# Optimization experiments

Measured on AMD Instinct MI355X. Metric: run time of the kernel, lower is better.

Reference implementation:

```python
import jax, jax.numpy as jnp
import numpy as np

B, T, D = 32, 2000, 1024

def setup_inputs() -> dict:
    key = jax.random.key(0)
    # drive with positive mean current so neurons actually spike
    I_seq = 100.0 * jax.random.normal(key, (B, T, D), dtype=jnp.float32) + 250.0
    C, g_L, E_L, V_T, Delta_T, tau_w = 200.0, 10.0, -70.0, -50.0, 2.0, 120.0
    a, b, R, V_reset, V_spike, dt = 0.0, 0.0, 1.0, -65.0, 30.0, 0.1
    tau_m = C / max(1e-06, g_L)
    params = jnp.array([tau_m, E_L, V_T, Delta_T, R, tau_w, a, b, V_reset, V_spike, dt],
                       dtype=jnp.float32)
    return {"I_seq": I_seq, "params": params}


def reference(I_seq, params):
    tau_m, E_L, V_T, Delta_T, R, tau_w, a, b, V_reset, V_spike, dt = params
    Bs, Ts, Ds = I_seq.shape
    # flatten to (T, B*D): scan over time, all neurons vectorized
    flat_I = jnp.transpose(I_seq, (1, 0, 2)).reshape(Ts, Bs * Ds)
    V0 = jnp.full((Bs * Ds,), E_L, dtype=I_seq.dtype)
    w0 = jnp.zeros((Bs * Ds,), dtype=I_seq.dtype)

    def step(carry, i_t):
        V, w = carry
        exp_term = Delta_T * jnp.exp((V - V_T) / Delta_T)
        dV = (-(V - E_L) + exp_term - R * w + R * i_t) / tau_m
        V = V + dt * dV
        dw = (a * (V - E_L) - w) / tau_w
        w = w + dt * dw
        spk = (V >= V_spike).astype(V.dtype)
        V = jnp.where(spk > 0.0, V_reset, V)
        w = jnp.where(spk > 0.0, w + b, w)
        return (V, w), spk

    (_, _), spikes = jax.lax.scan(step, (V0, w0), flat_I)  # spikes: (T, B*D)
    return jnp.transpose(spikes.reshape(Ts, Bs, Ds), (1, 0, 2))  # (B, T, D)
```

## Files before the change

kernel.cpp:

```cpp
#include <hip/hip_runtime.h>


#define Bn 32
#define Tn 2000
#define Dn 1024
#define NEUR (Bn * Dn)
#define UNR 16
#define NB (Tn / UNR)

#define EXP_LOG2EF 1.44269504088896341f
#define EXP_C1 0.693359375f
#define EXP_C2 -2.12194440e-4f
#define EXP_P0 1.9875691500e-4f
#define EXP_P1 1.3981999507e-3f
#define EXP_P2 8.3334519073e-3f
#define EXP_P3 4.1665795894e-2f
#define EXP_P4 1.6666665459e-1f
#define EXP_P5 5.0000001201e-1f

__device__ __forceinline__ float ref_expf(float x) {
    #pragma clang fp contract(off)
    float fx = __builtin_floorf(__builtin_fmaf(x, EXP_LOG2EF, 0.5f));
    float xr = __builtin_fmaf(fx, -EXP_C1, x);
    xr = __builtin_fmaf(fx, -EXP_C2, xr);
    float z2 = xr * xr;
    float y = EXP_P0;
    y = __builtin_fmaf(y, xr, EXP_P1);
    y = __builtin_fmaf(y, xr, EXP_P2);
    y = __builtin_fmaf(y, xr, EXP_P3);
    y = __builtin_fmaf(y, xr, EXP_P4);
    y = __builtin_fmaf(y, xr, EXP_P5);
    y = __builtin_fmaf(y, z2, xr);
    y = y + 1.0f;
    const int n = (int)fx;
    return y * __int_as_float((n + 127) << 23);
}

struct HP {
    float tau_m, rTM, dt, Vs, Vrst, E_L, V_T;
    float rDT;
    float KH;
    float T1C;
    float nC;
    int   kdt;
};

__device__ __forceinline__ float hot_step(float& V, float& t1, float& nEL,
                                          float i_t, const HP p) {
    #pragma clang fp contract(off)
    const float x  = t1 * p.rDT;
    const float fx = __builtin_floorf(__builtin_fmaf(t1, p.KH, 0.5f));
    float xr = __builtin_fmaf(fx, -EXP_C1, x);
    xr = __builtin_fmaf(fx, -EXP_C2, xr);
    const float z2 = xr * xr;
    float y = __builtin_fmaf(EXP_P0, xr, EXP_P1);
    y = __builtin_fmaf(y, xr, EXP_P2);
    y = __builtin_fmaf(y, xr, EXP_P3);
    y = __builtin_fmaf(y, xr, EXP_P4);
    y = __builtin_fmaf(y, xr, EXP_P5);
    y = __builtin_fmaf(y, z2, xr);
    y = y + 1.0f;
    const int   nsc = (int)fx;
    const float sc  = __int_as_float((nsc + 127 + p.kdt) << 23);
    const float et  = y * sc;
    float nm = nEL + et;
    nm = nm + i_t;
    const float q  = nm * p.rTM;
    const float er = __builtin_fmaf(-p.tau_m, q, nm);
    const float dV = __builtin_fmaf(er, p.rTM, q);
    const float Vp = __builtin_fmaf(p.dt, dV, V);
    const bool  s  = (Vp >= p.Vs);
    V   = s ? p.Vrst : Vp;
    t1  = s ? p.T1C  : (Vp - p.V_T);
    nEL = s ? p.nC   : (p.E_L - Vp);
    return s ? 1.0f : 0.0f;
}

__device__ __forceinline__ void step_simple(float& V, float i_t, float& spk_out,
                                            float E_L, float V_T, float Delta_T,
                                            float R, float tau_m, float V_spike,
                                            float V_reset, float dt) {
    #pragma clang fp contract(off)
    const float e  = ref_expf((V - V_T) / Delta_T);
    const float et = Delta_T * e;
    float nm = (-(V - E_L) + et);
    nm = nm + R * i_t;
    const float dV = nm / tau_m;
    V = __builtin_fmaf(dt, dV, V);
    spk_out = (V >= V_spike) ? 1.0f : 0.0f;
    V = (V >= V_spike) ? V_reset : V;
}

__device__ __forceinline__ void step_general(float& V, float& w, float i_t, float& spk_out,
                                             float E_L, float V_T, float Delta_T,
                                             float R, float tau_m, float tau_w,
                                             float a, float b,
                                             float V_spike, float V_reset, float dt) {
    #pragma clang fp contract(off)
    const float e  = ref_expf((V - V_T) / Delta_T);
    const float et = Delta_T * e;
    float nm = (-(V - E_L) + et);
    nm = __builtin_fmaf(-R, w, nm);
    nm = __builtin_fmaf(R, i_t, nm);
    const float dV = nm / tau_m;
    V = __builtin_fmaf(dt, dV, V);
    const float dwn = __builtin_fmaf(a, (V - E_L), -w);
    const float dw  = dwn / tau_w;
    w = __builtin_fmaf(dt, dw, w);
    spk_out = (V >= V_spike) ? 1.0f : 0.0f;
    const bool s = (V >= V_spike);
    V = s ? V_reset : V;
    w = s ? (w + b) : w;
}

#define RUN_BLOCKS(IPTR, OPTR, NBLK, ...) do {                                    \
    float bufA_[UNR], bufB_[UNR];                                                 \
    _Pragma("unroll") for (int k = 0; k < UNR; ++k) bufA_[k] = (IPTR)[k * Dn];    \
    for (int tb = 0; tb < (NBLK); tb += 2) {                                      \
        if (tb + 1 < (NBLK)) {                                                    \
            const float* pp_ = (IPTR) + (size_t)(tb + 1) * (UNR * Dn);            \
            _Pragma("unroll") for (int k = 0; k < UNR; ++k) bufB_[k] = pp_[k*Dn]; \
        }                                                                         \
        {                                                                         \
            float* oo_ = (OPTR) + (size_t)tb * (UNR * Dn);                        \
            _Pragma("unroll") for (int k = 0; k < UNR; ++k) {                     \
                const float i_t = bufA_[k];                                       \
                float* OSLOT = oo_ + (size_t)k * Dn; (void)OSLOT;                 \
                __VA_ARGS__;                                                      \
            }                                                                     \
        }                                                                         \
        if (tb + 2 < (NBLK)) {                                                    \
            const float* pp_ = (IPTR) + (size_t)(tb + 2) * (UNR * Dn);            \
            _Pragma("unroll") for (int k = 0; k < UNR; ++k) bufA_[k] = pp_[k*Dn]; \
        }                                                                         \
        if (tb + 1 < (NBLK)) {                                                    \
            float* oo_ = (OPTR) + (size_t)(tb + 1) * (UNR * Dn);                  \
            _Pragma("unroll") for (int k = 0; k < UNR; ++k) {                     \
                const float i_t = bufB_[k];                                       \
                float* OSLOT = oo_ + (size_t)k * Dn; (void)OSLOT;                 \
                __VA_ARGS__;                                                      \
            }                                                                     \
        }                                                                         \
    }                                                                             \
} while (0)

__launch_bounds__(128, 1)
__global__ void adex_kernel(const float* __restrict__ I,
                            const float* __restrict__ params,
                            float* __restrict__ out) {
    #pragma clang fp contract(off)

    const float tau_m   = params[0];
    const float E_L     = params[1];
    const float V_T     = params[2];
    const float Delta_T = params[3];
    const float R       = params[4];
    const float tau_w   = params[5];
    const float a       = params[6];
    const float b       = params[7];
    const float V_reset = params[8];
    const float V_spike = params[9];
    const float dt      = params[10];

    const int n = blockIdx.x * blockDim.x + threadIdx.x;
    if (n >= NEUR) return;
    const int bb = n >> 10;
    const int dd = n & (Dn - 1);

    const float* Ip = I   + (size_t)bb * (size_t)(Tn * Dn) + dd;
    float*       Op = out + (size_t)bb * (size_t)(Tn * Dn) + dd;

    const unsigned dtBits = __float_as_uint(Delta_T);
    const bool dtPow2 = ((dtBits & 0x7FFFFFu) == 0u) && Delta_T > 0.0f;
    const bool hot = (a == 0.0f) && (b == 0.0f) && (R == 1.0f) && dtPow2;

    float V = E_L;

    if (hot) {
        HP p;
        p.tau_m = tau_m;
        p.rTM   = 1.0f / tau_m;
        p.dt    = dt;
        p.Vs    = V_spike;
        p.Vrst  = V_reset;
        p.E_L   = E_L;
        p.V_T   = V_T;
        p.kdt   = (int)((dtBits >> 23) & 0xFFu) - 127;
        p.rDT   = 1.0f / Delta_T;
        p.KH    = EXP_LOG2EF * p.rDT;
        p.T1C   = V_reset - V_T;
        p.nC    = E_L - V_reset;

        float t1  = V - V_T;
        float nEL = E_L - V;
        RUN_BLOCKS(Ip, Op, NB,
            { *OSLOT = hot_step(V, t1, nEL, i_t, p); });
    } else if (a == 0.0f && b == 0.0f) {
        RUN_BLOCKS(Ip, Op, NB,
            { float spk; step_simple(V, i_t, spk, E_L, V_T, Delta_T, R, tau_m,
                                     V_spike, V_reset, dt); *OSLOT = spk; });
    } else {
        float w = 0.0f;
        RUN_BLOCKS(Ip, Op, NB,
            { float spk; step_general(V, w, i_t, spk, E_L, V_T, Delta_T, R, tau_m,
                                      tau_w, a, b, V_spike, V_reset, dt); *OSLOT = spk; });
    }
}

extern "C" void kernel_launch(void* const* d_in, const int* in_sizes, int n_in,
                              void* d_out, int out_size, void* d_ws, size_t ws_size,
                              hipStream_t stream) {
    const float* I      = (const float*)d_in[0];
    const float* params = (const float*)d_in[1];
    float*       out    = (float*)d_out;

    dim3 block(128);
    dim3 grid(NEUR / 128);
    adex_kernel<<<grid, block, 0, stream>>>(I, params, out);
}
```

Before: 190.2 us.

## Precompute post-reset step to shorten serial dependency chain in hot path

Restructures the hot-path recurrence so that the step following a spike uses a precomputed constant exponential term (the value at V_reset). The candidate post-reset voltage is computed in parallel with the general step, and a select picks between them. This takes the reset select off the critical path before the exp polynomial. It also inlines an explicit double-buffered prefetch of input blocks in place of the RUN_BLOCKS macro. The exp is still evaluated every step, so arithmetic work rises a little in exchange for a shorter dependency latency.

```diff
diff --git a/kernel.cpp b/kernel.cpp
--- a/kernel.cpp
+++ b/kernel.cpp
@@ -36,20 +36,10 @@
     return y * __int_as_float((n + 127) << 23);
 }
 
-struct HP {
-    float tau_m, rTM, dt, Vs, Vrst, E_L, V_T;
-    float rDT;
-    float KH;
-    float T1C;
-    float nC;
-    int   kdt;
-};
-
-__device__ __forceinline__ float hot_step(float& V, float& t1, float& nEL,
-                                          float i_t, const HP p) {
-    #pragma clang fp contract(off)
-    const float x  = t1 * p.rDT;
-    const float fx = __builtin_floorf(__builtin_fmaf(t1, p.KH, 0.5f));
+__device__ __forceinline__ float et_from_t1(float t1, float rDT, float KH, int kdt) {
+    #pragma clang fp contract(off)
+    const float x  = t1 * rDT;
+    const float fx = __builtin_floorf(__builtin_fmaf(t1, KH, 0.5f));
     float xr = __builtin_fmaf(fx, -EXP_C1, x);
     xr = __builtin_fmaf(fx, -EXP_C2, xr);
     const float z2 = xr * xr;
@@ -60,20 +50,8 @@
     y = __builtin_fmaf(y, xr, EXP_P5);
     y = __builtin_fmaf(y, z2, xr);
     y = y + 1.0f;
-    const int   nsc = (int)fx;
-    const float sc  = __int_as_float((nsc + 127 + p.kdt) << 23);
-    const float et  = y * sc;
-    float nm = nEL + et;
-    nm = nm + i_t;
-    const float q  = nm * p.rTM;
-    const float er = __builtin_fmaf(-p.tau_m, q, nm);
-    const float dV = __builtin_fmaf(er, p.rTM, q);
-    const float Vp = __builtin_fmaf(p.dt, dV, V);
-    const bool  s  = (Vp >= p.Vs);
-    V   = s ? p.Vrst : Vp;
-    t1  = s ? p.T1C  : (Vp - p.V_T);
-    nEL = s ? p.nC   : (p.E_L - Vp);
-    return s ? 1.0f : 0.0f;
+    const int nsc = (int)fx;
+    return y * __int_as_float((nsc + 127 + kdt) << 23);
 }
 
 __device__ __forceinline__ void step_simple(float& V, float i_t, float& spk_out,
@@ -174,28 +152,91 @@
     const bool dtPow2 = ((dtBits & 0x7FFFFFu) == 0u) && Delta_T > 0.0f;
     const bool hot = (a == 0.0f) && (b == 0.0f) && (R == 1.0f) && dtPow2;
 
+    if (hot) {
+        const int   kdt = (int)((dtBits >> 23) & 0xFFu) - 127;
+        const float rDT = 1.0f / Delta_T;
+        const float KH  = EXP_LOG2EF * rDT;
+        const float rTM = 1.0f / tau_m;
+        const float t1C  = V_reset - V_T;
+        const float etC  = et_from_t1(t1C, rDT, KH, kdt);
+        const float nC   = E_L - V_reset;
+        const float nmC0 = nC + etC;
+
+        float VP = E_L;
+        bool  s  = false;
+
+        float bufA[UNR], bufB[UNR], sp[UNR];
+        #pragma unroll
+        for (int k = 0; k < UNR; ++k) bufA[k] = Ip[k * Dn];
+
+        #define HOT_STEP(i_t, kk) do {                                            \
+                               \
+            const float nms = nmC0 + (i_t);                                       \
+            const float qs  = nms * rTM;                                          \
+            const float ers = __builtin_fmaf(-tau_m, qs, nms);                    \
+            const float dVs = __builtin_fmaf(ers, rTM, qs);                       \
+            const float Vs_ = __builtin_fmaf(dt, dVs, V_reset);                   \
+                  \
+            const float t1 = VP - V_T;                                            \
+            const float x  = t1 * rDT;                                            \
+            const float fx = __builtin_floorf(__builtin_fmaf(t1, KH, 0.5f));      \
+            float xr = __builtin_fmaf(fx, -EXP_C1, x);                            \
+            xr = __builtin_fmaf(fx, -EXP_C2, xr);                                 \
+            const float z2 = xr * xr;                                             \
+            float y = __builtin_fmaf(EXP_P0, xr, EXP_P1);                         \
+            y = __builtin_fmaf(y, xr, EXP_P2);                                    \
+            y = __builtin_fmaf(y, xr, EXP_P3);                                    \
+            y = __builtin_fmaf(y, xr, EXP_P4);                                    \
+            y = __builtin_fmaf(y, xr, EXP_P5);                                    \
+            y = __builtin_fmaf(y, z2, xr);                                        \
+            y = y + 1.0f;                                                         \
+            const int   nsc = (int)fx;                                            \
+            const float sc  = __int_as_float((nsc + 127 + kdt) << 23);            \
+            const float et  = y * sc;                                             \
+            const float nEL = E_L - VP;                                           \
+            float nm = nEL + et;                                                  \
+            nm = nm + (i_t);                                                      \
+            const float q  = nm * rTM;                                            \
+            const float er = __builtin_fmaf(-tau_m, q, nm);                       \
+            const float dV = __builtin_fmaf(er, rTM, q);                          \
+            const float Vns = __builtin_fmaf(dt, dV, VP);                         \
+            VP = s ? Vs_ : Vns;                       \
+            s  = (VP >= V_spike);               \
+            sp[kk] = s ? 1.0f : 0.0f;                                             \
+        } while (0)
+
+        for (int tb = 0; tb < NB; tb += 2) {
+            if (tb + 1 < NB) {
+                const float* p = Ip + (size_t)(tb + 1) * (UNR * Dn);
+                #pragma unroll
+                for (int k = 0; k < UNR; ++k) bufB[k] = p[k * Dn];
+            }
+            {
+                #pragma unroll
+                for (int k = 0; k < UNR; ++k) HOT_STEP(bufA[k], k);
+                float* o = Op + (size_t)tb * (UNR * Dn);
+                #pragma unroll
+                for (int k = 0; k < UNR; ++k) o[k * Dn] = sp[k];
+            }
+            if (tb + 2 < NB) {
+                const float* p = Ip + (size_t)(tb + 2) * (UNR * Dn);
+                #pragma unroll
+                for (int k = 0; k < UNR; ++k) bufA[k] = p[k * Dn];
+            }
+            if (tb + 1 < NB) {
+                #pragma unroll
+                for (int k = 0; k < UNR; ++k) HOT_STEP(bufB[k], k);
+                float* o = Op + (size_t)(tb + 1) * (UNR * Dn);
+                #pragma unroll
+                for (int k = 0; k < UNR; ++k) o[k * Dn] = sp[k];
+            }
+        }
+        #undef HOT_STEP
+        return;
+    }
+
     float V = E_L;
-
-    if (hot) {
-        HP p;
-        p.tau_m = tau_m;
-        p.rTM   = 1.0f / tau_m;
-        p.dt    = dt;
-        p.Vs    = V_spike;
-        p.Vrst  = V_reset;
-        p.E_L   = E_L;
-        p.V_T   = V_T;
-        p.kdt   = (int)((dtBits >> 23) & 0xFFu) - 127;
-        p.rDT   = 1.0f / Delta_T;
-        p.KH    = EXP_LOG2EF * p.rDT;
-        p.T1C   = V_reset - V_T;
-        p.nC    = E_L - V_reset;
-
-        float t1  = V - V_T;
-        float nEL = E_L - V;
-        RUN_BLOCKS(Ip, Op, NB,
-            { *OSLOT = hot_step(V, t1, nEL, i_t, p); });
-    } else if (a == 0.0f && b == 0.0f) {
+    if (a == 0.0f && b == 0.0f) {
         RUN_BLOCKS(Ip, Op, NB,
             { float spk; step_simple(V, i_t, spk, E_L, V_T, Delta_T, R, tau_m,
                                      V_spike, V_reset, dt); *OSLOT = spk; });
```

Measured after the change: 208.3 us. 9.6% more time.
